# Kernel optimization log

Hardware: AMD Instinct MI355X
Metric: run time of the kernel (lower is better)

The kernel has to match this reference:

```python
import jax, jax.numpy as jnp
import numpy as np

N_NODES = 20000
N_EDGES = 640000
D_IN = 128
D_HID = 128
N_LAYERS = 3


def setup_inputs() -> dict:
    key = jax.random.key(0)
    ks = jax.random.split(key, 2 + 4 * N_LAYERS)
    x = jax.random.normal(ks[0], (N_NODES, D_IN), dtype=jnp.float32)
    edge_index = jax.random.randint(ks[1], (2, N_EDGES), 0, N_NODES, dtype=jnp.int64)
    inp = {"x": x, "edge_index": edge_index}
    d_in = D_IN
    for l in range(N_LAYERS):
        s1 = 1.0 / np.sqrt(d_in)
        s2 = 1.0 / np.sqrt(D_HID)
        inp[f"w1_{l}"] = jax.random.uniform(ks[2 + 4 * l + 0], (d_in, D_HID), jnp.float32, -s1, s1)
        inp[f"b1_{l}"] = jax.random.uniform(ks[2 + 4 * l + 1], (D_HID,), jnp.float32, -s1, s1)
        inp[f"w2_{l}"] = jax.random.uniform(ks[2 + 4 * l + 2], (D_HID, D_HID), jnp.float32, -s2, s2)
        inp[f"b2_{l}"] = jax.random.uniform(ks[2 + 4 * l + 3], (D_HID,), jnp.float32, -s2, s2)
        d_in = D_HID
    return inp


def reference(x, edge_index, w1_0, b1_0, w2_0, b2_0,
              w1_1, b1_1, w2_1, b2_1, w1_2, b1_2, w2_2, b2_2):
    src = edge_index[0]
    dst = edge_index[1]
    n = x.shape[0]
    params = [(w1_0, b1_0, w2_0, b2_0), (w1_1, b1_1, w2_1, b2_1), (w1_2, b1_2, w2_2, b2_2)]
    z = x
    for w1, b1, w2, b2 in params:
        # GIN aggregation: (1 + eps) * x_i + sum_{j in N(i)} x_j, eps = 0
        agg = jax.ops.segment_sum(z[src], dst, num_segments=n)  # [N, D]
        h = z + agg
        # 2-layer MLP
        h = jax.nn.relu(h @ w1 + b1) @ w2 + b2
        # encoder activation
        z = jax.nn.relu(h)
    return z
```

## Files before the change

### kernel.cpp

```cpp
#include <hip/hip_runtime.h>

#define NN 20000
#define NE 640000
#define D  128
#define NDPAD 20480
#define CAP 96
#define NPX 2500
#define ECHUNK 2000

using short8 = __attribute__((ext_vector_type(8))) short;
using f32x4  = __attribute__((ext_vector_type(4))) float;

static __device__ __forceinline__ unsigned short f2bu(float f) {
  unsigned u = __float_as_uint(f);
  unsigned r = (u + 0x7fffu + ((u >> 16) & 1u)) >> 16;
  return (unsigned short)r;
}
static __device__ __forceinline__ unsigned packbf(float a, float b) {
  return (unsigned)f2bu(a) | ((unsigned)f2bu(b) << 16);
}
static __device__ __forceinline__ float bflo(unsigned u) { return __uint_as_float(u << 16); }
static __device__ __forceinline__ float bfhi(unsigned u) { return __uint_as_float(u & 0xffff0000u); }

#define ZB_BLK 80
#define CVT_BLK 2500
#define W_BLK 384
#define PREP_BLK (ZB_BLK + CVT_BLK + 1 + W_BLK)

__global__ __launch_bounds__(256) void prep_kernel(
    const float4* __restrict__ x, uint2* __restrict__ zbA, uint2* __restrict__ zbB,
    const float* __restrict__ wa, const float* __restrict__ wb,
    const float* __restrict__ wc, const float* __restrict__ wd,
    const float* __restrict__ we, const float* __restrict__ wf,
    unsigned short* __restrict__ wt_base,
    int* __restrict__ fill) {
  int b = blockIdx.x;
  int t = threadIdx.x;
  if (b < ZB_BLK) {
    fill[b * 256 + t] = 0;
  } else if (b < ZB_BLK + CVT_BLK) {
    int i = (b - ZB_BLK) * 256 + t;
    float4 v = x[i];
    zbA[i] = make_uint2(packbf(v.x, v.y), packbf(v.z, v.w));
  } else if (b == ZB_BLK + CVT_BLK) {
    if (t < 32)       zbA[NN * 32 + t] = make_uint2(0u, 0u);
    else if (t < 64)  zbB[NN * 32 + (t - 32)] = make_uint2(0u, 0u);
  } else {
    int wb_ = b - (ZB_BLK + CVT_BLK + 1);
    int widx = wb_ >> 6;
    const float* ws[6] = {wa, wb, wc, wd, we, wf};
    const float* w = ws[widx];
    unsigned short* wt = wt_base + (size_t)widx * D * D;
    int idx = (wb_ & 63) * 256 + t;
    int n = idx >> 7, k = idx & 127;
    wt[idx] = f2bu(w[k * D + n]);
  }
}

__global__ __launch_bounds__(256) void csr_kernel(const int* __restrict__ ei,
                                                  int* __restrict__ fill,
                                                  unsigned short* __restrict__ col_ell) {
  const int xcd = blockIdx.x & 7;
  const int chunk = blockIdx.x >> 3;
  const int nlo = xcd * NPX;
  const int nhi = nlo + NPX;
  const int e0 = chunk * ECHUNK;
  const int4* s4 = reinterpret_cast<const int4*>(ei + e0);
  const int4* d4 = reinterpret_cast<const int4*>(ei + NE + e0);
  for (int q = threadIdx.x; q < ECHUNK / 4; q += 256) {
    int4 d = d4[q];
    int4 s = s4[q];
    if (d.x >= nlo && d.x < nhi) {
      int p = atomicAdd(&fill[d.x], 1);
      if (p < CAP) col_ell[d.x * CAP + p] = (unsigned short)s.x;
    }
    if (d.y >= nlo && d.y < nhi) {
      int p = atomicAdd(&fill[d.y], 1);
      if (p < CAP) col_ell[d.y * CAP + p] = (unsigned short)s.y;
    }
    if (d.z >= nlo && d.z < nhi) {
      int p = atomicAdd(&fill[d.z], 1);
      if (p < CAP) col_ell[d.z * CAP + p] = (unsigned short)s.z;
    }
    if (d.w >= nlo && d.w < nhi) {
      int p = atomicAdd(&fill[d.w], 1);
      if (p < CAP) col_ell[d.w * CAP + p] = (unsigned short)s.w;
    }
  }
}

__global__ __launch_bounds__(512, 4) void layer_kernel(
    const uint4* __restrict__ zb4,
    const int* __restrict__ deg,
    const unsigned short* __restrict__ col_ell,
    const unsigned short* __restrict__ w1t,
    const float* __restrict__ b1,
    const unsigned short* __restrict__ w2t,
    const float* __restrict__ b2,
    unsigned short* __restrict__ zb_out,
    float* __restrict__ f_out) {
  __shared__ alignas(16) unsigned char Ht[16 * 256];
  __shared__ alignas(16) unsigned char H2[16 * 256];
  const int lane = threadIdx.x & 63;
  const int wv = threadIdx.x >> 6;
  const int nb = blockIdx.x * 16;
  const int hf = lane >> 4;
  const int cs = lane & 15;

  {
    const int r0 = wv * 2, r1 = r0 + 1;
    const int nodeA = __builtin_amdgcn_readfirstlane(nb + r0);
    const int nodeB = __builtin_amdgcn_readfirstlane(nb + r1);
    const int dgA = deg[nodeA], dgB = deg[nodeB];
    const unsigned short* cbA = col_ell + nodeA * CAP;
    const unsigned short* cbB = col_ell + nodeB * CAP;
    const int nch = (max(dgA, dgB) + 3) >> 2;
    float a0 = 0.f, a1 = 0.f, a2 = 0.f, a3 = 0.f;
    float a4 = 0.f, a5 = 0.f, a6 = 0.f, a7 = 0.f;
    float c0 = 0.f, c1 = 0.f, c2 = 0.f, c3 = 0.f;
    float c4 = 0.f, c5 = 0.f, c6 = 0.f, c7 = 0.f;
#pragma unroll 4
    for (int c = 0; c < nch; ++c) {
      int slot = c * 4 + hf;
      int idxA = (slot < dgA) ? (int)cbA[slot] : NN;
      int idxB = (slot < dgB) ? (int)cbB[slot] : NN;
      uint4 u = zb4[(size_t)idxA * 16 + cs];
      uint4 v = zb4[(size_t)idxB * 16 + cs];
      a0 += bflo(u.x); a1 += bfhi(u.x);
      a2 += bflo(u.y); a3 += bfhi(u.y);
      a4 += bflo(u.z); a5 += bfhi(u.z);
      a6 += bflo(u.w); a7 += bfhi(u.w);
      c0 += bflo(v.x); c1 += bfhi(v.x);
      c2 += bflo(v.y); c3 += bfhi(v.y);
      c4 += bflo(v.z); c5 += bfhi(v.z);
      c6 += bflo(v.w); c7 += bfhi(v.w);
    }
    a0 += __shfl_xor(a0, 16); a1 += __shfl_xor(a1, 16);
    a2 += __shfl_xor(a2, 16); a3 += __shfl_xor(a3, 16);
    a4 += __shfl_xor(a4, 16); a5 += __shfl_xor(a5, 16);
    a6 += __shfl_xor(a6, 16); a7 += __shfl_xor(a7, 16);
    c0 += __shfl_xor(c0, 16); c1 += __shfl_xor(c1, 16);
    c2 += __shfl_xor(c2, 16); c3 += __shfl_xor(c3, 16);
    c4 += __shfl_xor(c4, 16); c5 += __shfl_xor(c5, 16);
    c6 += __shfl_xor(c6, 16); c7 += __shfl_xor(c7, 16);
    a0 += __shfl_xor(a0, 32); a1 += __shfl_xor(a1, 32);
    a2 += __shfl_xor(a2, 32); a3 += __shfl_xor(a3, 32);
    a4 += __shfl_xor(a4, 32); a5 += __shfl_xor(a5, 32);
    a6 += __shfl_xor(a6, 32); a7 += __shfl_xor(a7, 32);
    c0 += __shfl_xor(c0, 32); c1 += __shfl_xor(c1, 32);
    c2 += __shfl_xor(c2, 32); c3 += __shfl_xor(c3, 32);
    c4 += __shfl_xor(c4, 32); c5 += __shfl_xor(c5, 32);
    c6 += __shfl_xor(c6, 32); c7 += __shfl_xor(c7, 32);
    uint4 sA = zb4[(size_t)nodeA * 16 + cs];
    uint4 sB = zb4[(size_t)nodeB * 16 + cs];
    a0 += bflo(sA.x); a1 += bfhi(sA.x);
    a2 += bflo(sA.y); a3 += bfhi(sA.y);
    a4 += bflo(sA.z); a5 += bfhi(sA.z);
    a6 += bflo(sA.w); a7 += bfhi(sA.w);
    c0 += bflo(sB.x); c1 += bfhi(sB.x);
    c2 += bflo(sB.y); c3 += bfhi(sB.y);
    c4 += bflo(sB.z); c5 += bfhi(sB.z);
    c6 += bflo(sB.w); c7 += bfhi(sB.w);
    if (hf == 0) {
      uint4 p;
      p.x = packbf(a0, a1); p.y = packbf(a2, a3);
      p.z = packbf(a4, a5); p.w = packbf(a6, a7);
      *reinterpret_cast<uint4*>(&Ht[(r0 * 256 + cs * 16) ^ ((r0 & 7) << 4)]) = p;
    } else if (hf == 1) {
      uint4 p;
      p.x = packbf(c0, c1); p.y = packbf(c2, c3);
      p.z = packbf(c4, c5); p.w = packbf(c6, c7);
      *reinterpret_cast<uint4*>(&Ht[(r1 * 256 + cs * 16) ^ ((r1 & 7) << 4)]) = p;
    }
  }
  __syncthreads();

  const int ar = lane & 15;
  const int kg = lane >> 4;
  const int crb = kg * 4;

  short8 a[4];
#pragma unroll
  for (int ks = 0; ks < 4; ++ks) {
    int byte = (ar * 256 + (ks * 32 + kg * 8) * 2) ^ ((ar & 7) << 4);
    a[ks] = *reinterpret_cast<const short8*>(&Ht[byte]);
  }
  f32x4 acc = (f32x4){0.f, 0.f, 0.f, 0.f};
#pragma unroll
  for (int ks = 0; ks < 4; ++ks) {
    short8 b = *reinterpret_cast<const short8*>(&w1t[(wv * 16 + ar) * D + ks * 32 + kg * 8]);
    acc = __builtin_amdgcn_mfma_f32_16x16x32_bf16(a[ks], b, acc, 0, 0, 0);
  }
  {
    int col = wv * 16 + ar;
    float bias = b1[col];
#pragma unroll
    for (int j = 0; j < 4; ++j) {
      int r = crb + j;
      float v = fmaxf(acc[j] + bias, 0.f);
      int byte = (r * 256 + col * 2) ^ ((r & 7) << 4);
      *reinterpret_cast<unsigned short*>(&H2[byte]) = f2bu(v);
    }
  }
  __syncthreads();

  short8 a2[4];
#pragma unroll
  for (int ks = 0; ks < 4; ++ks) {
    int byte = (ar * 256 + (ks * 32 + kg * 8) * 2) ^ ((ar & 7) << 4);
    a2[ks] = *reinterpret_cast<const short8*>(&H2[byte]);
  }
  acc = (f32x4){0.f, 0.f, 0.f, 0.f};
#pragma unroll
  for (int ks = 0; ks < 4; ++ks) {
    short8 b = *reinterpret_cast<const short8*>(&w2t[(wv * 16 + ar) * D + ks * 32 + kg * 8]);
    acc = __builtin_amdgcn_mfma_f32_16x16x32_bf16(a2[ks], b, acc, 0, 0, 0);
  }
  {
    int col = wv * 16 + ar;
    float bias = b2[col];
    if (f_out != nullptr) {
#pragma unroll
      for (int j = 0; j < 4; ++j) {
        int row = nb + crb + j;
        f_out[(size_t)row * D + col] = fmaxf(acc[j] + bias, 0.f);
      }
    } else {
#pragma unroll
      for (int j = 0; j < 4; ++j) {
        int row = nb + crb + j;
        zb_out[(size_t)row * D + col] = f2bu(fmaxf(acc[j] + bias, 0.f));
      }
    }
  }
}

extern "C" void kernel_launch(void* const* d_in, const int* in_sizes, int n_in,
                              void* d_out, int out_size, void* d_ws, size_t ws_size,
                              hipStream_t stream) {
  const float* x = (const float*)d_in[0];
  const int* ei = (const int*)d_in[1];
  const float* w1[3] = {(const float*)d_in[2], (const float*)d_in[6], (const float*)d_in[10]};
  const float* b1[3] = {(const float*)d_in[3], (const float*)d_in[7], (const float*)d_in[11]};
  const float* w2[3] = {(const float*)d_in[4], (const float*)d_in[8], (const float*)d_in[12]};
  const float* b2[3] = {(const float*)d_in[5], (const float*)d_in[9], (const float*)d_in[13]};
  float* out = (float*)d_out;

  char* wsb = (char*)d_ws;
  size_t off = 0;
  auto alloc = [&](size_t bytes) -> void* {
    void* p = wsb + off;
    off += (bytes + 255) & ~(size_t)255;
    return p;
  };
  unsigned short* zbA = (unsigned short*)alloc((size_t)(NN + 1) * D * 2);
  unsigned short* zbB = (unsigned short*)alloc((size_t)(NN + 1) * D * 2);
  unsigned short* wt  = (unsigned short*)alloc((size_t)6 * D * D * 2);
  int* fill = (int*)alloc((size_t)NDPAD * 4);
  unsigned short* col_ell = (unsigned short*)alloc((size_t)NDPAD * CAP * 2);

  prep_kernel<<<PREP_BLK, 256, 0, stream>>>(
      (const float4*)x, (uint2*)zbA, (uint2*)zbB, w1[0], w2[0], w1[1], w2[1], w1[2], w2[2],
      wt, fill);
  csr_kernel<<<(NE / ECHUNK) * 8, 256, 0, stream>>>(ei, fill, col_ell);

  const unsigned short* zin = zbA;
  unsigned short* zout = zbB;
  for (int l = 0; l < 3; ++l) {
    layer_kernel<<<NN / 16, 512, 0, stream>>>(
        (const uint4*)zin, fill, col_ell,
        wt + (size_t)(2 * l) * D * D, b1[l],
        wt + (size_t)(2 * l + 1) * D * D, b2[l],
        zout, (l == 2) ? out : nullptr);
    const unsigned short* t = zin;
    zin = zout;
    zout = (unsigned short*)t;
  }
}
```

Before: 152.7 us.

## Sort nodes by degree so blocks process similar-degree nodes together

Adds a single-block counting-sort kernel that orders nodes by descending in-degree, and makes the layer kernel map blocks and output rows through this permutation. Each wave handles two nodes and loops to the larger degree, so pairing nodes of similar degree is meant to cut wasted iterations, and heavy blocks get scheduled first to reduce tail imbalance. In exchange it adds a serial one-block kernel launch, an extra indirection load per row, and scattered output writes that lose the contiguous row layout.

```diff
diff --git a/kernel.cpp b/kernel.cpp
--- a/kernel.cpp
+++ b/kernel.cpp
@@ -89,10 +89,37 @@
   }
 }
 
+__global__ __launch_bounds__(1024) void order_kernel(const int* __restrict__ fill,
+                                                     int* __restrict__ order) {
+  __shared__ int hist[256];
+  __shared__ int base[256];
+  const int t = threadIdx.x;
+  if (t < 256) hist[t] = 0;
+  __syncthreads();
+  for (int i = t; i < NN; i += 1024) {
+    int d = min(fill[i], 255);
+    atomicAdd(&hist[d], 1);
+  }
+  __syncthreads();
+  if (t == 0) {
+    int acc = 0;
+    for (int b = 255; b >= 0; --b) { base[b] = acc; acc += hist[b]; }
+  }
+  __syncthreads();
+  if (t < 256) hist[t] = 0;
+  __syncthreads();
+  for (int i = t; i < NN; i += 1024) {
+    int d = min(fill[i], 255);
+    int pos = base[d] + atomicAdd(&hist[d], 1);
+    order[pos] = i;
+  }
+}
+
 __global__ __launch_bounds__(512, 4) void layer_kernel(
     const uint4* __restrict__ zb4,
     const int* __restrict__ deg,
     const unsigned short* __restrict__ col_ell,
+    const int* __restrict__ order,
     const unsigned short* __restrict__ w1t,
     const float* __restrict__ b1,
     const unsigned short* __restrict__ w2t,
@@ -109,8 +136,8 @@
 
   {
     const int r0 = wv * 2, r1 = r0 + 1;
-    const int nodeA = __builtin_amdgcn_readfirstlane(nb + r0);
-    const int nodeB = __builtin_amdgcn_readfirstlane(nb + r1);
+    const int nodeA = __builtin_amdgcn_readfirstlane(order[nb + r0]);
+    const int nodeB = __builtin_amdgcn_readfirstlane(order[nb + r1]);
     const int dgA = deg[nodeA], dgB = deg[nodeB];
     const unsigned short* cbA = col_ell + nodeA * CAP;
     const unsigned short* cbB = col_ell + nodeB * CAP;
@@ -222,13 +249,13 @@
     if (f_out != nullptr) {
 #pragma unroll
       for (int j = 0; j < 4; ++j) {
-        int row = nb + crb + j;
+        int row = order[nb + crb + j];
         f_out[(size_t)row * D + col] = fmaxf(acc[j] + bias, 0.f);
       }
     } else {
 #pragma unroll
       for (int j = 0; j < 4; ++j) {
-        int row = nb + crb + j;
+        int row = order[nb + crb + j];
         zb_out[(size_t)row * D + col] = f2bu(fmaxf(acc[j] + bias, 0.f));
       }
     }
@@ -258,17 +285,19 @@
   unsigned short* wt  = (unsigned short*)alloc((size_t)6 * D * D * 2);
   int* fill = (int*)alloc((size_t)NDPAD * 4);
   unsigned short* col_ell = (unsigned short*)alloc((size_t)NDPAD * CAP * 2);
+  int* order = (int*)alloc((size_t)NDPAD * 4);
 
   prep_kernel<<<PREP_BLK, 256, 0, stream>>>(
       (const float4*)x, (uint2*)zbA, (uint2*)zbB, w1[0], w2[0], w1[1], w2[1], w1[2], w2[2],
       wt, fill);
   csr_kernel<<<(NE / ECHUNK) * 8, 256, 0, stream>>>(ei, fill, col_ell);
+  order_kernel<<<1, 1024, 0, stream>>>(fill, order);
 
   const unsigned short* zin = zbA;
   unsigned short* zout = zbB;
   for (int l = 0; l < 3; ++l) {
     layer_kernel<<<NN / 16, 512, 0, stream>>>(
-        (const uint4*)zin, fill, col_ell,
+        (const uint4*)zin, fill, col_ell, order,
         wt + (size_t)(2 * l) * D * D, b1[l],
         wt + (size_t)(2 * l + 1) * D * D, b2[l],
         zout, (l == 2) ? out : nullptr);
```

After: 175.8 us. +15.1%, slower.

## Fuse prep, CSR build and three GIN layers into one persistent kernel

Applied to the files above, without the earlier changes.

Replaces five kernel launches with a tiny init kernel plus one persistent mega-kernel of 496 blocks that uses atomic-counter grid barriers between phases (prep, ELL build, each layer). Layer tiles are handed out dynamically through an atomic work counter. The aim is to remove launch gaps and tail effects between kernels. In exchange it relies on every block being co-resident for the spin barriers to avoid deadlock, and it pays for atomic tile fetches and the barrier spins themselves.

```diff
diff --git a/kernel.cpp b/kernel.cpp
--- a/kernel.cpp
+++ b/kernel.cpp
@@ -6,7 +6,11 @@
 #define NDPAD 20480
 #define CAP 96
 #define NPX 2500
-#define ECHUNK 2000
+#define NB 496
+#define NT 512
+#define NCHUNK 64
+#define EC 10000
+#define NTILE 1250
 
 using short8 = __attribute__((ext_vector_type(8))) short;
 using f32x4  = __attribute__((ext_vector_type(4))) float;
@@ -22,216 +26,255 @@
 static __device__ __forceinline__ float bflo(unsigned u) { return __uint_as_float(u << 16); }
 static __device__ __forceinline__ float bfhi(unsigned u) { return __uint_as_float(u & 0xffff0000u); }
 
-#define ZB_BLK 80
-#define CVT_BLK 2500
-#define W_BLK 384
-#define PREP_BLK (ZB_BLK + CVT_BLK + 1 + W_BLK)
-
-__global__ __launch_bounds__(256) void prep_kernel(
-    const float4* __restrict__ x, uint2* __restrict__ zbA, uint2* __restrict__ zbB,
+__global__ __launch_bounds__(64) void init_kernel(int* __restrict__ sync) {
+  if (threadIdx.x < 16) sync[threadIdx.x] = 0;
+}
+
+static __device__ __forceinline__ void gbar(int* __restrict__ sync, int slot) {
+  __syncthreads();
+  if (threadIdx.x == 0) {
+    __threadfence();
+    int old = atomicAdd(&sync[slot], 1);
+    if (old == NB - 1) {
+      atomicExch(&sync[6 + slot], 1);
+    } else {
+      while (atomicAdd(&sync[6 + slot], 0) == 0) __builtin_amdgcn_s_sleep(8);
+    }
+    __threadfence();
+  }
+  __syncthreads();
+}
+
+__global__ __launch_bounds__(512, 4) void mega_kernel(
+    const float4* __restrict__ x,
+    const int* __restrict__ ei,
     const float* __restrict__ wa, const float* __restrict__ wb,
     const float* __restrict__ wc, const float* __restrict__ wd,
     const float* __restrict__ we, const float* __restrict__ wf,
-    unsigned short* __restrict__ wt_base,
-    int* __restrict__ fill) {
-  int b = blockIdx.x;
-  int t = threadIdx.x;
-  if (b < ZB_BLK) {
-    fill[b * 256 + t] = 0;
-  } else if (b < ZB_BLK + CVT_BLK) {
-    int i = (b - ZB_BLK) * 256 + t;
-    float4 v = x[i];
-    zbA[i] = make_uint2(packbf(v.x, v.y), packbf(v.z, v.w));
-  } else if (b == ZB_BLK + CVT_BLK) {
-    if (t < 32)       zbA[NN * 32 + t] = make_uint2(0u, 0u);
-    else if (t < 64)  zbB[NN * 32 + (t - 32)] = make_uint2(0u, 0u);
-  } else {
-    int wb_ = b - (ZB_BLK + CVT_BLK + 1);
-    int widx = wb_ >> 6;
-    const float* ws[6] = {wa, wb, wc, wd, we, wf};
-    const float* w = ws[widx];
-    unsigned short* wt = wt_base + (size_t)widx * D * D;
-    int idx = (wb_ & 63) * 256 + t;
-    int n = idx >> 7, k = idx & 127;
-    wt[idx] = f2bu(w[k * D + n]);
-  }
-}
-
-__global__ __launch_bounds__(256) void csr_kernel(const int* __restrict__ ei,
-                                                  int* __restrict__ fill,
-                                                  unsigned short* __restrict__ col_ell) {
-  const int xcd = blockIdx.x & 7;
-  const int chunk = blockIdx.x >> 3;
-  const int nlo = xcd * NPX;
-  const int nhi = nlo + NPX;
-  const int e0 = chunk * ECHUNK;
-  const int4* s4 = reinterpret_cast<const int4*>(ei + e0);
-  const int4* d4 = reinterpret_cast<const int4*>(ei + NE + e0);
-  for (int q = threadIdx.x; q < ECHUNK / 4; q += 256) {
-    int4 d = d4[q];
-    int4 s = s4[q];
-    if (d.x >= nlo && d.x < nhi) {
-      int p = atomicAdd(&fill[d.x], 1);
-      if (p < CAP) col_ell[d.x * CAP + p] = (unsigned short)s.x;
-    }
-    if (d.y >= nlo && d.y < nhi) {
-      int p = atomicAdd(&fill[d.y], 1);
-      if (p < CAP) col_ell[d.y * CAP + p] = (unsigned short)s.y;
-    }
-    if (d.z >= nlo && d.z < nhi) {
-      int p = atomicAdd(&fill[d.z], 1);
-      if (p < CAP) col_ell[d.z * CAP + p] = (unsigned short)s.z;
-    }
-    if (d.w >= nlo && d.w < nhi) {
-      int p = atomicAdd(&fill[d.w], 1);
-      if (p < CAP) col_ell[d.w * CAP + p] = (unsigned short)s.w;
-    }
-  }
-}
-
-__global__ __launch_bounds__(512, 4) void layer_kernel(
-    const uint4* __restrict__ zb4,
-    const int* __restrict__ deg,
-    const unsigned short* __restrict__ col_ell,
-    const unsigned short* __restrict__ w1t,
-    const float* __restrict__ b1,
-    const unsigned short* __restrict__ w2t,
-    const float* __restrict__ b2,
-    unsigned short* __restrict__ zb_out,
-    float* __restrict__ f_out) {
+    const float* __restrict__ b1_0, const float* __restrict__ b2_0,
+    const float* __restrict__ b1_1, const float* __restrict__ b2_1,
+    const float* __restrict__ b1_2, const float* __restrict__ b2_2,
+    unsigned short* __restrict__ zbA, unsigned short* __restrict__ zbB,
+    unsigned short* __restrict__ wt,
+    int* __restrict__ fill,
+    unsigned short* __restrict__ col_ell,
+    int* __restrict__ sync,
+    float* __restrict__ out) {
   __shared__ alignas(16) unsigned char Ht[16 * 256];
   __shared__ alignas(16) unsigned char H2[16 * 256];
+  __shared__ int sTile;
+
+  const int gtid = blockIdx.x * NT + threadIdx.x;
+  const int gsz = NB * NT;
+
+  {
+    for (int i = gtid; i < NDPAD; i += gsz) fill[i] = 0;
+    uint2* zA2 = reinterpret_cast<uint2*>(zbA);
+    for (int i = gtid; i < NE; i += gsz) {
+      float4 v = x[i];
+      zA2[i] = make_uint2(packbf(v.x, v.y), packbf(v.z, v.w));
+    }
+    if (gtid < 32) {
+      reinterpret_cast<uint2*>(zbA)[NN * 32 + gtid] = make_uint2(0u, 0u);
+    } else if (gtid < 64) {
+      reinterpret_cast<uint2*>(zbB)[NN * 32 + (gtid - 32)] = make_uint2(0u, 0u);
+    }
+    const float* ws[6] = {wa, wb, wc, wd, we, wf};
+    for (int i = gtid; i < 6 * D * D; i += gsz) {
+      int widx = i >> 14;
+      int idx = i & 16383;
+      int n = idx >> 7, k = idx & 127;
+      wt[(size_t)widx * D * D + idx] = f2bu(ws[widx][k * D + n]);
+    }
+  }
+  gbar(sync, 0);
+
+  {
+    const int xcd = blockIdx.x & 7;
+    const int nlo = xcd * NPX;
+    const int nhi = nlo + NPX;
+    for (int c = blockIdx.x >> 3; c < NCHUNK; c += NB >> 3) {
+      const int e0 = c * EC;
+      const int4* s4 = reinterpret_cast<const int4*>(ei + e0);
+      const int4* d4 = reinterpret_cast<const int4*>(ei + NE + e0);
+      for (int q = threadIdx.x; q < EC / 4; q += NT) {
+        int4 d = d4[q];
+        int4 s = s4[q];
+        if (d.x >= nlo && d.x < nhi) {
+          int p = atomicAdd(&fill[d.x], 1);
+          if (p < CAP) col_ell[d.x * CAP + p] = (unsigned short)s.x;
+        }
+        if (d.y >= nlo && d.y < nhi) {
+          int p = atomicAdd(&fill[d.y], 1);
+          if (p < CAP) col_ell[d.y * CAP + p] = (unsigned short)s.y;
+        }
+        if (d.z >= nlo && d.z < nhi) {
+          int p = atomicAdd(&fill[d.z], 1);
+          if (p < CAP) col_ell[d.z * CAP + p] = (unsigned short)s.z;
+        }
+        if (d.w >= nlo && d.w < nhi) {
+          int p = atomicAdd(&fill[d.w], 1);
+          if (p < CAP) col_ell[d.w * CAP + p] = (unsigned short)s.w;
+        }
+      }
+    }
+  }
+  gbar(sync, 1);
+
   const int lane = threadIdx.x & 63;
   const int wv = threadIdx.x >> 6;
-  const int nb = blockIdx.x * 16;
   const int hf = lane >> 4;
   const int cs = lane & 15;
-
-  {
-    const int r0 = wv * 2, r1 = r0 + 1;
-    const int nodeA = __builtin_amdgcn_readfirstlane(nb + r0);
-    const int nodeB = __builtin_amdgcn_readfirstlane(nb + r1);
-    const int dgA = deg[nodeA], dgB = deg[nodeB];
-    const unsigned short* cbA = col_ell + nodeA * CAP;
-    const unsigned short* cbB = col_ell + nodeB * CAP;
-    const int nch = (max(dgA, dgB) + 3) >> 2;
-    float a0 = 0.f, a1 = 0.f, a2 = 0.f, a3 = 0.f;
-    float a4 = 0.f, a5 = 0.f, a6 = 0.f, a7 = 0.f;
-    float c0 = 0.f, c1 = 0.f, c2 = 0.f, c3 = 0.f;
-    float c4 = 0.f, c5 = 0.f, c6 = 0.f, c7 = 0.f;
-#pragma unroll 4
-    for (int c = 0; c < nch; ++c) {
-      int slot = c * 4 + hf;
-      int idxA = (slot < dgA) ? (int)cbA[slot] : NN;
-      int idxB = (slot < dgB) ? (int)cbB[slot] : NN;
-      uint4 u = zb4[(size_t)idxA * 16 + cs];
-      uint4 v = zb4[(size_t)idxB * 16 + cs];
-      a0 += bflo(u.x); a1 += bfhi(u.x);
-      a2 += bflo(u.y); a3 += bfhi(u.y);
-      a4 += bflo(u.z); a5 += bfhi(u.z);
-      a6 += bflo(u.w); a7 += bfhi(u.w);
-      c0 += bflo(v.x); c1 += bfhi(v.x);
-      c2 += bflo(v.y); c3 += bfhi(v.y);
-      c4 += bflo(v.z); c5 += bfhi(v.z);
-      c6 += bflo(v.w); c7 += bfhi(v.w);
-    }
-    a0 += __shfl_xor(a0, 16); a1 += __shfl_xor(a1, 16);
-    a2 += __shfl_xor(a2, 16); a3 += __shfl_xor(a3, 16);
-    a4 += __shfl_xor(a4, 16); a5 += __shfl_xor(a5, 16);
-    a6 += __shfl_xor(a6, 16); a7 += __shfl_xor(a7, 16);
-    c0 += __shfl_xor(c0, 16); c1 += __shfl_xor(c1, 16);
-    c2 += __shfl_xor(c2, 16); c3 += __shfl_xor(c3, 16);
-    c4 += __shfl_xor(c4, 16); c5 += __shfl_xor(c5, 16);
-    c6 += __shfl_xor(c6, 16); c7 += __shfl_xor(c7, 16);
-    a0 += __shfl_xor(a0, 32); a1 += __shfl_xor(a1, 32);
-    a2 += __shfl_xor(a2, 32); a3 += __shfl_xor(a3, 32);
-    a4 += __shfl_xor(a4, 32); a5 += __shfl_xor(a5, 32);
-    a6 += __shfl_xor(a6, 32); a7 += __shfl_xor(a7, 32);
-    c0 += __shfl_xor(c0, 32); c1 += __shfl_xor(c1, 32);
-    c2 += __shfl_xor(c2, 32); c3 += __shfl_xor(c3, 32);
-    c4 += __shfl_xor(c4, 32); c5 += __shfl_xor(c5, 32);
-    c6 += __shfl_xor(c6, 32); c7 += __shfl_xor(c7, 32);
-    uint4 sA = zb4[(size_t)nodeA * 16 + cs];
-    uint4 sB = zb4[(size_t)nodeB * 16 + cs];
-    a0 += bflo(sA.x); a1 += bfhi(sA.x);
-    a2 += bflo(sA.y); a3 += bfhi(sA.y);
-    a4 += bflo(sA.z); a5 += bfhi(sA.z);
-    a6 += bflo(sA.w); a7 += bfhi(sA.w);
-    c0 += bflo(sB.x); c1 += bfhi(sB.x);
-    c2 += bflo(sB.y); c3 += bfhi(sB.y);
-    c4 += bflo(sB.z); c5 += bfhi(sB.z);
-    c6 += bflo(sB.w); c7 += bfhi(sB.w);
-    if (hf == 0) {
-      uint4 p;
-      p.x = packbf(a0, a1); p.y = packbf(a2, a3);
-      p.z = packbf(a4, a5); p.w = packbf(a6, a7);
-      *reinterpret_cast<uint4*>(&Ht[(r0 * 256 + cs * 16) ^ ((r0 & 7) << 4)]) = p;
-    } else if (hf == 1) {
-      uint4 p;
-      p.x = packbf(c0, c1); p.y = packbf(c2, c3);
-      p.z = packbf(c4, c5); p.w = packbf(c6, c7);
-      *reinterpret_cast<uint4*>(&Ht[(r1 * 256 + cs * 16) ^ ((r1 & 7) << 4)]) = p;
-    }
-  }
-  __syncthreads();
-
   const int ar = lane & 15;
   const int kg = lane >> 4;
   const int crb = kg * 4;
-
-  short8 a[4];
-#pragma unroll
-  for (int ks = 0; ks < 4; ++ks) {
-    int byte = (ar * 256 + (ks * 32 + kg * 8) * 2) ^ ((ar & 7) << 4);
-    a[ks] = *reinterpret_cast<const short8*>(&Ht[byte]);
-  }
-  f32x4 acc = (f32x4){0.f, 0.f, 0.f, 0.f};
-#pragma unroll
-  for (int ks = 0; ks < 4; ++ks) {
-    short8 b = *reinterpret_cast<const short8*>(&w1t[(wv * 16 + ar) * D + ks * 32 + kg * 8]);
-    acc = __builtin_amdgcn_mfma_f32_16x16x32_bf16(a[ks], b, acc, 0, 0, 0);
-  }
-  {
-    int col = wv * 16 + ar;
-    float bias = b1[col];
-#pragma unroll
-    for (int j = 0; j < 4; ++j) {
-      int r = crb + j;
-      float v = fmaxf(acc[j] + bias, 0.f);
-      int byte = (r * 256 + col * 2) ^ ((r & 7) << 4);
-      *reinterpret_cast<unsigned short*>(&H2[byte]) = f2bu(v);
-    }
-  }
-  __syncthreads();
-
-  short8 a2[4];
-#pragma unroll
-  for (int ks = 0; ks < 4; ++ks) {
-    int byte = (ar * 256 + (ks * 32 + kg * 8) * 2) ^ ((ar & 7) << 4);
-    a2[ks] = *reinterpret_cast<const short8*>(&H2[byte]);
-  }
-  acc = (f32x4){0.f, 0.f, 0.f, 0.f};
-#pragma unroll
-  for (int ks = 0; ks < 4; ++ks) {
-    short8 b = *reinterpret_cast<const short8*>(&w2t[(wv * 16 + ar) * D + ks * 32 + kg * 8]);
-    acc = __builtin_amdgcn_mfma_f32_16x16x32_bf16(a2[ks], b, acc, 0, 0, 0);
-  }
-  {
-    int col = wv * 16 + ar;
-    float bias = b2[col];
-    if (f_out != nullptr) {
-#pragma unroll
-      for (int j = 0; j < 4; ++j) {
-        int row = nb + crb + j;
-        f_out[(size_t)row * D + col] = fmaxf(acc[j] + bias, 0.f);
-      }
-    } else {
-#pragma unroll
-      for (int j = 0; j < 4; ++j) {
-        int row = nb + crb + j;
-        zb_out[(size_t)row * D + col] = f2bu(fmaxf(acc[j] + bias, 0.f));
-      }
-    }
+  const float* b1s[3] = {b1_0, b1_1, b1_2};
+  const float* b2s[3] = {b2_0, b2_1, b2_2};
+
+  const unsigned short* zin = zbA;
+  unsigned short* zout = zbB;
+  for (int l = 0; l < 3; ++l) {
+    const uint4* zb4 = reinterpret_cast<const uint4*>(zin);
+    const unsigned short* w1t = wt + (size_t)(2 * l) * D * D;
+    const unsigned short* w2t = wt + (size_t)(2 * l + 1) * D * D;
+    const float* b1 = b1s[l];
+    const float* b2 = b2s[l];
+    const bool last = (l == 2);
+    for (;;) {
+      if (threadIdx.x == 0) sTile = atomicAdd(&sync[12 + l], 1);
+      __syncthreads();
+      const int tile = sTile;
+      if (tile >= NTILE) break;
+      const int nb = tile * 16;
+
+      {
+        const int r0 = wv * 2, r1 = r0 + 1;
+        const int nodeA = __builtin_amdgcn_readfirstlane(nb + r0);
+        const int nodeB = __builtin_amdgcn_readfirstlane(nb + r1);
+        const int dgA = fill[nodeA], dgB = fill[nodeB];
+        const unsigned short* cbA = col_ell + nodeA * CAP;
+        const unsigned short* cbB = col_ell + nodeB * CAP;
+        const int nch = (max(dgA, dgB) + 3) >> 2;
+        float a0 = 0.f, a1 = 0.f, a2 = 0.f, a3 = 0.f;
+        float a4 = 0.f, a5 = 0.f, a6 = 0.f, a7 = 0.f;
+        float c0 = 0.f, c1 = 0.f, c2 = 0.f, c3 = 0.f;
+        float c4 = 0.f, c5 = 0.f, c6 = 0.f, c7 = 0.f;
+#pragma unroll 4
+        for (int c = 0; c < nch; ++c) {
+          int slot = c * 4 + hf;
+          int idxA = (slot < dgA) ? (int)cbA[slot] : NN;
+          int idxB = (slot < dgB) ? (int)cbB[slot] : NN;
+          uint4 u = zb4[(size_t)idxA * 16 + cs];
+          uint4 v = zb4[(size_t)idxB * 16 + cs];
+          a0 += bflo(u.x); a1 += bfhi(u.x);
+          a2 += bflo(u.y); a3 += bfhi(u.y);
+          a4 += bflo(u.z); a5 += bfhi(u.z);
+          a6 += bflo(u.w); a7 += bfhi(u.w);
+          c0 += bflo(v.x); c1 += bfhi(v.x);
+          c2 += bflo(v.y); c3 += bfhi(v.y);
+          c4 += bflo(v.z); c5 += bfhi(v.z);
+          c6 += bflo(v.w); c7 += bfhi(v.w);
+        }
+        a0 += __shfl_xor(a0, 16); a1 += __shfl_xor(a1, 16);
+        a2 += __shfl_xor(a2, 16); a3 += __shfl_xor(a3, 16);
+        a4 += __shfl_xor(a4, 16); a5 += __shfl_xor(a5, 16);
+        a6 += __shfl_xor(a6, 16); a7 += __shfl_xor(a7, 16);
+        c0 += __shfl_xor(c0, 16); c1 += __shfl_xor(c1, 16);
+        c2 += __shfl_xor(c2, 16); c3 += __shfl_xor(c3, 16);
+        c4 += __shfl_xor(c4, 16); c5 += __shfl_xor(c5, 16);
+        c6 += __shfl_xor(c6, 16); c7 += __shfl_xor(c7, 16);
+        a0 += __shfl_xor(a0, 32); a1 += __shfl_xor(a1, 32);
+        a2 += __shfl_xor(a2, 32); a3 += __shfl_xor(a3, 32);
+        a4 += __shfl_xor(a4, 32); a5 += __shfl_xor(a5, 32);
+        a6 += __shfl_xor(a6, 32); a7 += __shfl_xor(a7, 32);
+        c0 += __shfl_xor(c0, 32); c1 += __shfl_xor(c1, 32);
+        c2 += __shfl_xor(c2, 32); c3 += __shfl_xor(c3, 32);
+        c4 += __shfl_xor(c4, 32); c5 += __shfl_xor(c5, 32);
+        c6 += __shfl_xor(c6, 32); c7 += __shfl_xor(c7, 32);
+        uint4 sA = zb4[(size_t)nodeA * 16 + cs];
+        uint4 sB = zb4[(size_t)nodeB * 16 + cs];
+        a0 += bflo(sA.x); a1 += bfhi(sA.x);
+        a2 += bflo(sA.y); a3 += bfhi(sA.y);
+        a4 += bflo(sA.z); a5 += bfhi(sA.z);
+        a6 += bflo(sA.w); a7 += bfhi(sA.w);
+        c0 += bflo(sB.x); c1 += bfhi(sB.x);
+        c2 += bflo(sB.y); c3 += bfhi(sB.y);
+        c4 += bflo(sB.z); c5 += bfhi(sB.z);
+        c6 += bflo(sB.w); c7 += bfhi(sB.w);
+        if (hf == 0) {
+          uint4 p;
+          p.x = packbf(a0, a1); p.y = packbf(a2, a3);
+          p.z = packbf(a4, a5); p.w = packbf(a6, a7);
+          *reinterpret_cast<uint4*>(&Ht[(r0 * 256 + cs * 16) ^ ((r0 & 7) << 4)]) = p;
+        } else if (hf == 1) {
+          uint4 p;
+          p.x = packbf(c0, c1); p.y = packbf(c2, c3);
+          p.z = packbf(c4, c5); p.w = packbf(c6, c7);
+          *reinterpret_cast<uint4*>(&Ht[(r1 * 256 + cs * 16) ^ ((r1 & 7) << 4)]) = p;
+        }
+      }
+      __syncthreads();
+
+      short8 a[4];
+#pragma unroll
+      for (int ks = 0; ks < 4; ++ks) {
+        int byte = (ar * 256 + (ks * 32 + kg * 8) * 2) ^ ((ar & 7) << 4);
+        a[ks] = *reinterpret_cast<const short8*>(&Ht[byte]);
+      }
+      f32x4 acc = (f32x4){0.f, 0.f, 0.f, 0.f};
+#pragma unroll
+      for (int ks = 0; ks < 4; ++ks) {
+        short8 b = *reinterpret_cast<const short8*>(&w1t[(wv * 16 + ar) * D + ks * 32 + kg * 8]);
+        acc = __builtin_amdgcn_mfma_f32_16x16x32_bf16(a[ks], b, acc, 0, 0, 0);
+      }
+      {
+        int col = wv * 16 + ar;
+        float bias = b1[col];
+#pragma unroll
+        for (int j = 0; j < 4; ++j) {
+          int r = crb + j;
+          float v = fmaxf(acc[j] + bias, 0.f);
+          int byte = (r * 256 + col * 2) ^ ((r & 7) << 4);
+          *reinterpret_cast<unsigned short*>(&H2[byte]) = f2bu(v);
+        }
+      }
+      __syncthreads();
+
+      short8 a2[4];
+#pragma unroll
+      for (int ks = 0; ks < 4; ++ks) {
+        int byte = (ar * 256 + (ks * 32 + kg * 8) * 2) ^ ((ar & 7) << 4);
+        a2[ks] = *reinterpret_cast<const short8*>(&H2[byte]);
+      }
+      acc = (f32x4){0.f, 0.f, 0.f, 0.f};
+#pragma unroll
+      for (int ks = 0; ks < 4; ++ks) {
+        short8 b = *reinterpret_cast<const short8*>(&w2t[(wv * 16 + ar) * D + ks * 32 + kg * 8]);
+        acc = __builtin_amdgcn_mfma_f32_16x16x32_bf16(a2[ks], b, acc, 0, 0, 0);
+      }
+      {
+        int col = wv * 16 + ar;
+        float bias = b2[col];
+        if (last) {
+#pragma unroll
+          for (int j = 0; j < 4; ++j) {
+            int row = nb + crb + j;
+            out[(size_t)row * D + col] = fmaxf(acc[j] + bias, 0.f);
+          }
+        } else {
+#pragma unroll
+          for (int j = 0; j < 4; ++j) {
+            int row = nb + crb + j;
+            zout[(size_t)row * D + col] = f2bu(fmaxf(acc[j] + bias, 0.f));
+          }
+        }
+      }
+      __syncthreads();
+    }
+    if (l < 2) gbar(sync, 2 + l);
+    const unsigned short* t = zin;
+    zin = zout;
+    zout = (unsigned short*)t;
   }
 }
 
@@ -258,22 +301,12 @@
   unsigned short* wt  = (unsigned short*)alloc((size_t)6 * D * D * 2);
   int* fill = (int*)alloc((size_t)NDPAD * 4);
   unsigned short* col_ell = (unsigned short*)alloc((size_t)NDPAD * CAP * 2);
-
-  prep_kernel<<<PREP_BLK, 256, 0, stream>>>(
-      (const float4*)x, (uint2*)zbA, (uint2*)zbB, w1[0], w2[0], w1[1], w2[1], w1[2], w2[2],
-      wt, fill);
-  csr_kernel<<<(NE / ECHUNK) * 8, 256, 0, stream>>>(ei, fill, col_ell);
-
-  const unsigned short* zin = zbA;
-  unsigned short* zout = zbB;
-  for (int l = 0; l < 3; ++l) {
-    layer_kernel<<<NN / 16, 512, 0, stream>>>(
-        (const uint4*)zin, fill, col_ell,
-        wt + (size_t)(2 * l) * D * D, b1[l],
-        wt + (size_t)(2 * l + 1) * D * D, b2[l],
-        zout, (l == 2) ? out : nullptr);
-    const unsigned short* t = zin;
-    zin = zout;
-    zout = (unsigned short*)t;
-  }
-}
+  int* sync = (int*)alloc((size_t)64 * 4);
+
+  init_kernel<<<1, 64, 0, stream>>>(sync);
+  mega_kernel<<<NB, NT, 0, stream>>>(
+      (const float4*)x, ei,
+      w1[0], w2[0], w1[1], w2[1], w1[2], w2[2],
+      b1[0], b2[0], b1[1], b2[1], b1[2], b2[2],
+      zbA, zbB, wt, fill, col_ell, sync, out);
+}
```

New measurement: 450.4 us. 195% more time.

## Split GIN layer into per-half-feature aggregation kernels and separate MLP kernel

Applied to the files above, without the earlier changes.

Replaces the fused aggregate+MLP layer kernel with two aggregation launches that each gather half of the feature columns (64 of 128) into a global H buffer, followed by an MLP kernel that reads H from global memory. The intent is to shrink the gather working set per pass so neighbor rows stay cache-resident. In exchange it adds an extra global write/read of the aggregated features, re-reads the adjacency lists twice, and triples kernel launches per layer.

```diff
diff --git a/kernel.cpp b/kernel.cpp
--- a/kernel.cpp
+++ b/kernel.cpp
@@ -89,92 +89,74 @@
   }
 }
 
-__global__ __launch_bounds__(512, 4) void layer_kernel(
-    const uint4* __restrict__ zb4,
+__global__ __launch_bounds__(512, 4) void agg_kernel(
+    const uint2* __restrict__ zb2,
     const int* __restrict__ deg,
     const unsigned short* __restrict__ col_ell,
+    const int h,
+    unsigned short* __restrict__ Hrow) {
+  const int lane = threadIdx.x & 63;
+  const int wv = threadIdx.x >> 6;
+  const int nb = blockIdx.x * 16;
+  const int hf = lane >> 4;
+  const int cs = lane & 15;
+  const int r0 = wv * 2, r1 = r0 + 1;
+  const int nodeA = __builtin_amdgcn_readfirstlane(nb + r0);
+  const int nodeB = __builtin_amdgcn_readfirstlane(nb + r1);
+  const int dgA = deg[nodeA], dgB = deg[nodeB];
+  const unsigned short* cbA = col_ell + nodeA * CAP;
+  const unsigned short* cbB = col_ell + nodeB * CAP;
+  const int nch = (max(dgA, dgB) + 3) >> 2;
+  const int co = h * 16 + cs;
+  float a0 = 0.f, a1 = 0.f, a2 = 0.f, a3 = 0.f;
+  float c0 = 0.f, c1 = 0.f, c2 = 0.f, c3 = 0.f;
+#pragma unroll 8
+  for (int c = 0; c < nch; ++c) {
+    int slot = c * 4 + hf;
+    int idxA = (slot < dgA) ? (int)cbA[slot] : NN;
+    int idxB = (slot < dgB) ? (int)cbB[slot] : NN;
+    uint2 u = zb2[(size_t)idxA * 32 + co];
+    uint2 v = zb2[(size_t)idxB * 32 + co];
+    a0 += bflo(u.x); a1 += bfhi(u.x);
+    a2 += bflo(u.y); a3 += bfhi(u.y);
+    c0 += bflo(v.x); c1 += bfhi(v.x);
+    c2 += bflo(v.y); c3 += bfhi(v.y);
+  }
+  a0 += __shfl_xor(a0, 16); a1 += __shfl_xor(a1, 16);
+  a2 += __shfl_xor(a2, 16); a3 += __shfl_xor(a3, 16);
+  c0 += __shfl_xor(c0, 16); c1 += __shfl_xor(c1, 16);
+  c2 += __shfl_xor(c2, 16); c3 += __shfl_xor(c3, 16);
+  a0 += __shfl_xor(a0, 32); a1 += __shfl_xor(a1, 32);
+  a2 += __shfl_xor(a2, 32); a3 += __shfl_xor(a3, 32);
+  c0 += __shfl_xor(c0, 32); c1 += __shfl_xor(c1, 32);
+  c2 += __shfl_xor(c2, 32); c3 += __shfl_xor(c3, 32);
+  uint2 sA = zb2[(size_t)nodeA * 32 + co];
+  uint2 sB = zb2[(size_t)nodeB * 32 + co];
+  a0 += bflo(sA.x); a1 += bfhi(sA.x);
+  a2 += bflo(sA.y); a3 += bfhi(sA.y);
+  c0 += bflo(sB.x); c1 += bfhi(sB.x);
+  c2 += bflo(sB.y); c3 += bfhi(sB.y);
+  if (hf == 0) {
+    uint2 p = make_uint2(packbf(a0, a1), packbf(a2, a3));
+    *reinterpret_cast<uint2*>(&Hrow[(size_t)nodeA * D + h * 64 + cs * 4]) = p;
+  } else if (hf == 1) {
+    uint2 p = make_uint2(packbf(c0, c1), packbf(c2, c3));
+    *reinterpret_cast<uint2*>(&Hrow[(size_t)nodeB * D + h * 64 + cs * 4]) = p;
+  }
+}
+
+__global__ __launch_bounds__(512, 4) void mlp_kernel(
+    const unsigned short* __restrict__ Hrow,
     const unsigned short* __restrict__ w1t,
     const float* __restrict__ b1,
     const unsigned short* __restrict__ w2t,
     const float* __restrict__ b2,
     unsigned short* __restrict__ zb_out,
     float* __restrict__ f_out) {
-  __shared__ alignas(16) unsigned char Ht[16 * 256];
   __shared__ alignas(16) unsigned char H2[16 * 256];
   const int lane = threadIdx.x & 63;
   const int wv = threadIdx.x >> 6;
   const int nb = blockIdx.x * 16;
-  const int hf = lane >> 4;
-  const int cs = lane & 15;
-
-  {
-    const int r0 = wv * 2, r1 = r0 + 1;
-    const int nodeA = __builtin_amdgcn_readfirstlane(nb + r0);
-    const int nodeB = __builtin_amdgcn_readfirstlane(nb + r1);
-    const int dgA = deg[nodeA], dgB = deg[nodeB];
-    const unsigned short* cbA = col_ell + nodeA * CAP;
-    const unsigned short* cbB = col_ell + nodeB * CAP;
-    const int nch = (max(dgA, dgB) + 3) >> 2;
-    float a0 = 0.f, a1 = 0.f, a2 = 0.f, a3 = 0.f;
-    float a4 = 0.f, a5 = 0.f, a6 = 0.f, a7 = 0.f;
-    float c0 = 0.f, c1 = 0.f, c2 = 0.f, c3 = 0.f;
-    float c4 = 0.f, c5 = 0.f, c6 = 0.f, c7 = 0.f;
-#pragma unroll 4
-    for (int c = 0; c < nch; ++c) {
-      int slot = c * 4 + hf;
-      int idxA = (slot < dgA) ? (int)cbA[slot] : NN;
-      int idxB = (slot < dgB) ? (int)cbB[slot] : NN;
-      uint4 u = zb4[(size_t)idxA * 16 + cs];
-      uint4 v = zb4[(size_t)idxB * 16 + cs];
-      a0 += bflo(u.x); a1 += bfhi(u.x);
-      a2 += bflo(u.y); a3 += bfhi(u.y);
-      a4 += bflo(u.z); a5 += bfhi(u.z);
-      a6 += bflo(u.w); a7 += bfhi(u.w);
-      c0 += bflo(v.x); c1 += bfhi(v.x);
-      c2 += bflo(v.y); c3 += bfhi(v.y);
-      c4 += bflo(v.z); c5 += bfhi(v.z);
-      c6 += bflo(v.w); c7 += bfhi(v.w);
-    }
-    a0 += __shfl_xor(a0, 16); a1 += __shfl_xor(a1, 16);
-    a2 += __shfl_xor(a2, 16); a3 += __shfl_xor(a3, 16);
-    a4 += __shfl_xor(a4, 16); a5 += __shfl_xor(a5, 16);
-    a6 += __shfl_xor(a6, 16); a7 += __shfl_xor(a7, 16);
-    c0 += __shfl_xor(c0, 16); c1 += __shfl_xor(c1, 16);
-    c2 += __shfl_xor(c2, 16); c3 += __shfl_xor(c3, 16);
-    c4 += __shfl_xor(c4, 16); c5 += __shfl_xor(c5, 16);
-    c6 += __shfl_xor(c6, 16); c7 += __shfl_xor(c7, 16);
-    a0 += __shfl_xor(a0, 32); a1 += __shfl_xor(a1, 32);
-    a2 += __shfl_xor(a2, 32); a3 += __shfl_xor(a3, 32);
-    a4 += __shfl_xor(a4, 32); a5 += __shfl_xor(a5, 32);
-    a6 += __shfl_xor(a6, 32); a7 += __shfl_xor(a7, 32);
-    c0 += __shfl_xor(c0, 32); c1 += __shfl_xor(c1, 32);
-    c2 += __shfl_xor(c2, 32); c3 += __shfl_xor(c3, 32);
-    c4 += __shfl_xor(c4, 32); c5 += __shfl_xor(c5, 32);
-    c6 += __shfl_xor(c6, 32); c7 += __shfl_xor(c7, 32);
-    uint4 sA = zb4[(size_t)nodeA * 16 + cs];
-    uint4 sB = zb4[(size_t)nodeB * 16 + cs];
-    a0 += bflo(sA.x); a1 += bfhi(sA.x);
-    a2 += bflo(sA.y); a3 += bfhi(sA.y);
-    a4 += bflo(sA.z); a5 += bfhi(sA.z);
-    a6 += bflo(sA.w); a7 += bfhi(sA.w);
-    c0 += bflo(sB.x); c1 += bfhi(sB.x);
-    c2 += bflo(sB.y); c3 += bfhi(sB.y);
-    c4 += bflo(sB.z); c5 += bfhi(sB.z);
-    c6 += bflo(sB.w); c7 += bfhi(sB.w);
-    if (hf == 0) {
-      uint4 p;
-      p.x = packbf(a0, a1); p.y = packbf(a2, a3);
-      p.z = packbf(a4, a5); p.w = packbf(a6, a7);
-      *reinterpret_cast<uint4*>(&Ht[(r0 * 256 + cs * 16) ^ ((r0 & 7) << 4)]) = p;
-    } else if (hf == 1) {
-      uint4 p;
-      p.x = packbf(c0, c1); p.y = packbf(c2, c3);
-      p.z = packbf(c4, c5); p.w = packbf(c6, c7);
-      *reinterpret_cast<uint4*>(&Ht[(r1 * 256 + cs * 16) ^ ((r1 & 7) << 4)]) = p;
-    }
-  }
-  __syncthreads();
-
   const int ar = lane & 15;
   const int kg = lane >> 4;
   const int crb = kg * 4;
@@ -182,8 +164,7 @@
   short8 a[4];
 #pragma unroll
   for (int ks = 0; ks < 4; ++ks) {
-    int byte = (ar * 256 + (ks * 32 + kg * 8) * 2) ^ ((ar & 7) << 4);
-    a[ks] = *reinterpret_cast<const short8*>(&Ht[byte]);
+    a[ks] = *reinterpret_cast<const short8*>(&Hrow[(size_t)(nb + ar) * D + ks * 32 + kg * 8]);
   }
   f32x4 acc = (f32x4){0.f, 0.f, 0.f, 0.f};
 #pragma unroll
@@ -258,6 +239,7 @@
   unsigned short* wt  = (unsigned short*)alloc((size_t)6 * D * D * 2);
   int* fill = (int*)alloc((size_t)NDPAD * 4);
   unsigned short* col_ell = (unsigned short*)alloc((size_t)NDPAD * CAP * 2);
+  unsigned short* Hbuf = (unsigned short*)alloc((size_t)NN * D * 2);
 
   prep_kernel<<<PREP_BLK, 256, 0, stream>>>(
       (const float4*)x, (uint2*)zbA, (uint2*)zbB, w1[0], w2[0], w1[1], w2[1], w1[2], w2[2],
@@ -267,8 +249,12 @@
   const unsigned short* zin = zbA;
   unsigned short* zout = zbB;
   for (int l = 0; l < 3; ++l) {
-    layer_kernel<<<NN / 16, 512, 0, stream>>>(
-        (const uint4*)zin, fill, col_ell,
+    agg_kernel<<<NN / 16, 512, 0, stream>>>(
+        (const uint2*)zin, fill, col_ell, 0, Hbuf);
+    agg_kernel<<<NN / 16, 512, 0, stream>>>(
+        (const uint2*)zin, fill, col_ell, 1, Hbuf);
+    mlp_kernel<<<NN / 16, 512, 0, stream>>>(
+        Hbuf,
         wt + (size_t)(2 * l) * D * D, b1[l],
         wt + (size_t)(2 * l + 1) * D * D, b2[l],
         zout, (l == 2) ? out : nullptr);
```

Result: slower. 199.2 us (+30.4%).
